# Optimization experiments

Measured on AMD Instinct MI355X. Metric: run time of the kernel, lower is better.

Reference implementation:

```python
import jax, jax.numpy as jnp
import numpy as np


def setup_inputs() -> dict:
    key = jax.random.key(0)
    k1, k2 = jax.random.split(key)
    x = jax.random.normal(k1, (32, 112, 112, 128), dtype=jnp.float32)
    # Conv2D kernel: HWIO layout, 7x7, in=2 (mean,max), out=1
    W = jax.random.normal(k2, (7, 7, 2, 1), dtype=jnp.float32) * 0.1
    b = jnp.zeros((1,), dtype=jnp.float32)
    return {"x": x, "W": W, "b": b}


def reference(x, W, b):
    # channel statistics (NHWC, reduce over channel axis)
    mean = jnp.mean(x, axis=-1, keepdims=True)          # [B,H,W,1]
    mx = jnp.max(x, axis=-1, keepdims=True)             # [B,H,W,1]
    merged = jnp.concatenate([mean, mx], axis=-1)       # [B,H,W,2]
    # small 7x7 conv, 'same' padding, 1 output channel
    attn = jax.lax.conv_general_dilated(
        merged, W,
        window_strides=(1, 1),
        padding="SAME",
        dimension_numbers=("NHWC", "HWIO", "NHWC"),
    ) + b                                                 # [B,H,W,1]
    gate = jax.nn.sigmoid(attn)
    return x * gate                                       # broadcast multiply
```

## Files before the change

kernel.cpp:

```cpp
#include <hip/hip_runtime.h>

static constexpr int Bn = 32;
static constexpr int Hn = 112;
static constexpr int Wn = 112;
static constexpr int Cn = 128;
static constexpr int NPIX = Bn * Hn * Wn;
static constexpr int HALO = 3;

typedef float floatx4 __attribute__((ext_vector_type(4)));

__global__ __launch_bounds__(256) void stats_kernel(const float* __restrict__ x,
                                                    float2* __restrict__ stats) {
    const int tid  = blockIdx.x * blockDim.x + threadIdx.x;
    const int pix  = tid >> 5;
    const int lane = tid & 31;
    const floatx4* __restrict__ x4 = reinterpret_cast<const floatx4*>(x);

    floatx4 v = x4[(size_t)pix * 32 + lane];
    float s = v.x + v.y + v.z + v.w;
    float m = fmaxf(fmaxf(v.x, v.y), fmaxf(v.z, v.w));

#pragma unroll
    for (int off = 16; off >= 1; off >>= 1) {
        s += __shfl_xor(s, off);
        m = fmaxf(m, __shfl_xor(m, off));
    }
    if (lane == 0) {
        stats[pix] = make_float2(s * (1.0f / 128.0f), m);
    }
}

__global__ __launch_bounds__(256) void conv_mul_kernel(const float* __restrict__ x,
                                                       const float2* __restrict__ stats,
                                                       const float* __restrict__ Wc,
                                                       const float* __restrict__ bias,
                                                       float* __restrict__ out) {
    __shared__ float2 sdat[7][Wn + 2 * HALO];
    __shared__ float  glds[Wn];
    __shared__ float  w[98];

    const int tid = threadIdx.x;
    const int r   = blockIdx.x % Hn;
    const int b   = blockIdx.x / Hn;

    if (tid < 98) w[tid] = Wc[tid];
    for (int i = tid; i < 7 * (Wn + 2 * HALO); i += 256)
        ((float2*)sdat)[i] = make_float2(0.f, 0.f);
    __syncthreads();

    for (int p = tid; p < 7 * Wn; p += 256) {
        const int kr = p / Wn;
        const int c  = p % Wn;
        const int rr = r - HALO + kr;
        if (rr >= 0 && rr < Hn)
            sdat[kr][c + HALO] = stats[(size_t)(b * Hn + rr) * Wn + c];
    }
    __syncthreads();

    if (tid < Wn) {
        float acc = bias[0];
#pragma unroll
        for (int kh = 0; kh < 7; ++kh)
#pragma unroll
            for (int kw = 0; kw < 7; ++kw) {
                const float2 sv = sdat[kh][tid + kw];
                acc = fmaf(sv.x, w[(kh * 7 + kw) * 2 + 0], acc);
                acc = fmaf(sv.y, w[(kh * 7 + kw) * 2 + 1], acc);
            }
        glds[tid] = 1.0f / (1.0f + expf(-acc));
    }
    __syncthreads();

    const floatx4* __restrict__ x4 = reinterpret_cast<const floatx4*>(x);
    floatx4* __restrict__ o4 = reinterpret_cast<floatx4*>(out);
    const size_t base = ((size_t)(b * Hn + r) * Wn) * 32;
#pragma unroll 2
    for (int i = tid; i < Wn * 32; i += 256) {
        const float g = glds[i >> 5];
        floatx4 v = x4[base + i];
        v *= g;
        __builtin_nontemporal_store(v, &o4[base + i]);
    }
}

extern "C" void kernel_launch(void* const* d_in, const int* in_sizes, int n_in,
                              void* d_out, int out_size, void* d_ws, size_t ws_size,
                              hipStream_t stream) {
    const float* x  = (const float*)d_in[0];
    const float* Wc = (const float*)d_in[1];
    const float* bb = (const float*)d_in[2];
    float* out = (float*)d_out;

    float2* stats = (float2*)d_ws;

    stats_kernel<<<(NPIX * 32) / 256, 256, 0, stream>>>(x, stats);
    conv_mul_kernel<<<Bn * Hn, 256, 0, stream>>>(x, stats, Wc, bb, out);
}
```

Before: 102.6 us.

## Fuse channel stats into conv-gate kernel with halo recomputation and row swizzle

Removes the separate stats kernel and its workspace. Each block now recomputes mean and max for its own row and the six neighbouring halo rows directly from x, keeps its own row in registers, and reuses those registers for the final gated multiply. The intent is to avoid a second full HBM read of x and one kernel launch. In exchange, each block reads seven rows, relying on cache hits for the halo rows, and block-to-row mapping is swizzled across XCDs.

```diff
diff --git a/kernel.cpp b/kernel.cpp
--- a/kernel.cpp
+++ b/kernel.cpp
@@ -3,57 +3,72 @@
 static constexpr int Bn = 32;
 static constexpr int Hn = 112;
 static constexpr int Wn = 112;
-static constexpr int Cn = 128;
-static constexpr int NPIX = Bn * Hn * Wn;
 static constexpr int HALO = 3;
+static constexpr int NROWS = Bn * Hn;
 
 typedef float floatx4 __attribute__((ext_vector_type(4)));
 
-__global__ __launch_bounds__(256) void stats_kernel(const float* __restrict__ x,
-                                                    float2* __restrict__ stats) {
-    const int tid  = blockIdx.x * blockDim.x + threadIdx.x;
-    const int pix  = tid >> 5;
-    const int lane = tid & 31;
-    const floatx4* __restrict__ x4 = reinterpret_cast<const floatx4*>(x);
-
-    floatx4 v = x4[(size_t)pix * 32 + lane];
-    float s = v.x + v.y + v.z + v.w;
-    float m = fmaxf(fmaxf(v.x, v.y), fmaxf(v.z, v.w));
-
-#pragma unroll
-    for (int off = 16; off >= 1; off >>= 1) {
-        s += __shfl_xor(s, off);
-        m = fmaxf(m, __shfl_xor(m, off));
-    }
-    if (lane == 0) {
-        stats[pix] = make_float2(s * (1.0f / 128.0f), m);
-    }
-}
-
-__global__ __launch_bounds__(256) void conv_mul_kernel(const float* __restrict__ x,
-                                                       const float2* __restrict__ stats,
-                                                       const float* __restrict__ Wc,
-                                                       const float* __restrict__ bias,
-                                                       float* __restrict__ out) {
+__global__ __launch_bounds__(256) void fused_row_kernel(const float* __restrict__ x,
+                                                        const float* __restrict__ Wc,
+                                                        const float* __restrict__ bias,
+                                                        float* __restrict__ out) {
     __shared__ float2 sdat[7][Wn + 2 * HALO];
     __shared__ float  glds[Wn];
     __shared__ float  w[98];
 
-    const int tid = threadIdx.x;
-    const int r   = blockIdx.x % Hn;
-    const int b   = blockIdx.x / Hn;
+    const int work = (blockIdx.x & 7) * (NROWS / 8) + (blockIdx.x >> 3);
+    const int b = work / Hn;
+    const int r = work % Hn;
+
+    const int tid  = threadIdx.x;
+    const int lane = tid & 31;
+    const int grp  = tid >> 5;
 
     if (tid < 98) w[tid] = Wc[tid];
     for (int i = tid; i < 7 * (Wn + 2 * HALO); i += 256)
         ((float2*)sdat)[i] = make_float2(0.f, 0.f);
     __syncthreads();
 
-    for (int p = tid; p < 7 * Wn; p += 256) {
-        const int kr = p / Wn;
-        const int c  = p % Wn;
-        const int rr = r - HALO + kr;
-        if (rr >= 0 && rr < Hn)
-            sdat[kr][c + HALO] = stats[(size_t)(b * Hn + rr) * Wn + c];
+    const floatx4* __restrict__ x4 = reinterpret_cast<const floatx4*>(x);
+    const size_t imgbase = (size_t)b * Hn * Wn * 32;
+
+    floatx4 xv[14];
+#pragma unroll
+    for (int j = 0; j < 14; ++j) {
+        const int c = grp + 8 * j;
+        xv[j] = x4[imgbase + ((size_t)r * Wn + c) * 32 + lane];
+    }
+
+#pragma unroll
+    for (int j = 0; j < 14; ++j) {
+        const int c = grp + 8 * j;
+        const floatx4 v = xv[j];
+        float s = v.x + v.y + v.z + v.w;
+        float m = fmaxf(fmaxf(v.x, v.y), fmaxf(v.z, v.w));
+#pragma unroll
+        for (int off = 16; off >= 1; off >>= 1) {
+            s += __shfl_xor(s, off);
+            m = fmaxf(m, __shfl_xor(m, off));
+        }
+        if (lane == 0) sdat[HALO][c + HALO] = make_float2(s * (1.0f / 128.0f), m);
+    }
+
+    for (int p = grp; p < 6 * Wn; p += 8) {
+        const int kr0 = p / Wn;
+        const int kr  = kr0 + (kr0 >= HALO);
+        const int c   = p % Wn;
+        const int rr  = r - HALO + kr;
+        if (rr >= 0 && rr < Hn) {
+            const floatx4 v = x4[imgbase + ((size_t)rr * Wn + c) * 32 + lane];
+            float s = v.x + v.y + v.z + v.w;
+            float m = fmaxf(fmaxf(v.x, v.y), fmaxf(v.z, v.w));
+#pragma unroll
+            for (int off = 16; off >= 1; off >>= 1) {
+                s += __shfl_xor(s, off);
+                m = fmaxf(m, __shfl_xor(m, off));
+            }
+            if (lane == 0) sdat[kr][c + HALO] = make_float2(s * (1.0f / 128.0f), m);
+        }
     }
     __syncthreads();
 
@@ -71,15 +86,13 @@
     }
     __syncthreads();
 
-    const floatx4* __restrict__ x4 = reinterpret_cast<const floatx4*>(x);
     floatx4* __restrict__ o4 = reinterpret_cast<floatx4*>(out);
-    const size_t base = ((size_t)(b * Hn + r) * Wn) * 32;
-#pragma unroll 2
-    for (int i = tid; i < Wn * 32; i += 256) {
-        const float g = glds[i >> 5];
-        floatx4 v = x4[base + i];
-        v *= g;
-        __builtin_nontemporal_store(v, &o4[base + i]);
+#pragma unroll
+    for (int j = 0; j < 14; ++j) {
+        const int c = grp + 8 * j;
+        floatx4 v = xv[j];
+        v *= glds[c];
+        __builtin_nontemporal_store(v, &o4[imgbase + ((size_t)r * Wn + c) * 32 + lane]);
     }
 }
 
@@ -91,8 +104,5 @@
     const float* bb = (const float*)d_in[2];
     float* out = (float*)d_out;
 
-    float2* stats = (float2*)d_ws;
-
-    stats_kernel<<<(NPIX * 32) / 256, 256, 0, stream>>>(x, stats);
-    conv_mul_kernel<<<Bn * Hn, 256, 0, stream>>>(x, stats, Wc, bb, out);
+    fused_row_kernel<<<NROWS, 256, 0, stream>>>(x, Wc, bb, out);
 }
```

Result: slower. 226.1 us (+120.4%).
